# Kernel optimization log

Measured on AMD Instinct MI355X. Metric: run time of the kernel, lower is better.

Reference implementation:

```python
import jax, jax.numpy as jnp
import numpy as np

BLOCK = 128  # fp8 weight block size (128, 128)

def dequant_block_fp8(w, scale_inv, block=BLOCK):
    # w: [E, N, K] fp8 values (simulated in f32); scale_inv: [E, N//block, K//block]
    E, N, K = w.shape
    wb = w.reshape(E, N // block, block, K // block, block)
    wb = wb * scale_inv[:, :, None, :, None]
    return wb.reshape(E, N, K)

def setup_inputs() -> dict:
    E, T, H, I, TOPK = 8, 256, 2048, 1024, 2
    key = jax.random.key(0)
    ks = jax.random.split(key, 6)
    x = jax.random.normal(ks[0], (T, H), dtype=jnp.float32)
    topk_ids = jax.random.randint(ks[1], (T, TOPK), 0, E, dtype=jnp.int64)
    topk_weights = jax.random.uniform(ks[2], (T, TOPK), dtype=jnp.float32)
    # fused gate+up projection: [E, 2I, H]; down projection: [E, H, I]
    w13_fp8 = jax.random.normal(ks[3], (E, 2 * I, H), dtype=jnp.float32) * 0.05
    w13_scale = jax.random.uniform(ks[4], (E, 2 * I // BLOCK, H // BLOCK), dtype=jnp.float32, minval=0.5, maxval=1.5)
    w2_fp8 = jax.random.normal(ks[5], (E, H, I), dtype=jnp.float32) * 0.05
    w2_scale = jax.random.uniform(jax.random.fold_in(key, 7), (E, H // BLOCK, I // BLOCK), dtype=jnp.float32, minval=0.5, maxval=1.5)
    return {
        "x": x, "topk_ids": topk_ids, "topk_weights": topk_weights,
        "w13_fp8": w13_fp8, "w13_scale": w13_scale,
        "w2_fp8": w2_fp8, "w2_scale": w2_scale,
        "moe_n_slice": 1, "n_expert_slice": 8, "ep_shift": 0,
    }

def reference(x, topk_ids, topk_weights, w13_fp8, w13_scale, w2_fp8, w2_scale,
              moe_n_slice, n_expert_slice, ep_shift):
    T, H = x.shape
    E = w13_fp8.shape[0]
    I = w2_fp8.shape[2]
    # per-expert block-FP8 dequant (the redundant dequant the kernel should fuse)
    w13 = dequant_block_fp8(w13_fp8, w13_scale)  # [E, 2I, H]
    w2 = dequant_block_fp8(w2_fp8, w2_scale)     # [E, H, I]
    # SwiGLU expert MLP computed for all experts, combined by routing weights
    gate_up = jnp.einsum('th,enh->ten', x, w13)  # [T, E, 2I]
    gate, up = gate_up[..., :I], gate_up[..., I:]
    act = jax.nn.silu(gate) * up                 # [T, E, I]
    y = jnp.einsum('tei,ehi->teh', act, w2)      # [T, E, H]
    # dense combine matrix equivalent to routed top-k dispatch
    combine = jnp.zeros((T, E), x.dtype).at[jnp.arange(T)[:, None], topk_ids].add(topk_weights.astype(x.dtype))
    return jnp.einsum('teh,te->th', y, combine)
```

## Files before the change

kernel.cpp:

```cpp
#include <hip/hip_runtime.h>
#include <cstdint>

#define NEXP 8
#define NTOK 256
#define NSLOT 512
#define HD 2048
#define ID 1024

typedef short bf16x8 __attribute__((ext_vector_type(8)));
typedef float f32x4  __attribute__((ext_vector_type(4)));

__global__ __launch_bounds__(256) void route_k(const int* __restrict__ ids,
                                               int* __restrict__ counts,
                                               int* __restrict__ slots) {
  int tid = threadIdx.x;
  if (tid < NEXP) counts[tid] = 0;
  __syncthreads();
  for (int s = tid; s < NSLOT; s += 256) {
    int e = ids[s];
    int pos = atomicAdd(&counts[e], 1);
    slots[e * NSLOT + pos] = s;
  }
}

__device__ __forceinline__ void split4(float x, float y, float z, float w,
                                       uint2& hi, uint2& lo) {
  uint32_t u0 = __float_as_uint(x), u1 = __float_as_uint(y),
           u2 = __float_as_uint(z), u3 = __float_as_uint(w);
  uint32_t h0 = u0 & 0xFFFF0000u, h1 = u1 & 0xFFFF0000u;
  uint32_t h2 = u2 & 0xFFFF0000u, h3 = u3 & 0xFFFF0000u;
  hi.x = (u0 >> 16) | h1;
  hi.y = (u2 >> 16) | h3;
  float l0 = x - __uint_as_float(h0), l1 = y - __uint_as_float(h1);
  float l2 = z - __uint_as_float(h2), l3 = w - __uint_as_float(h3);
  lo.x = (__float_as_uint(l0) >> 16) | (__float_as_uint(l1) & 0xFFFF0000u);
  lo.y = (__float_as_uint(l2) >> 16) | (__float_as_uint(l3) & 0xFFFF0000u);
}

template <int K, int ASHIFT>
__global__ __launch_bounds__(256, 2) void moe_gemm_mfma(
    const float* __restrict__ A, int lda,
    const float* __restrict__ B, int64_t bstride,
    const float* __restrict__ Sc, int sstride_e, int sstride_n,
    float* __restrict__ C, int ldc,
    const int* __restrict__ counts, const int* __restrict__ slots) {
  constexpr int NT = K / 32;
  const int e = blockIdx.z;
  const int cnt = counts[e];
  const int mbase = blockIdx.y * 64;
  if (mbase >= cnt) return;
  const int n0 = blockIdx.x * 64;

  __shared__ ushort Ah[2][64][32], Al[2][64][32];
  __shared__ ushort Bh[2][64][32], Bl[2][64][32];
  __shared__ int s_slots[64];

  const int tid = threadIdx.x;
  const int lane = tid & 63;
  const int wave = tid >> 6;
  const int wm = wave >> 1;
  const int wn = wave & 1;

  const int* sl = slots + e * NSLOT;
  if (tid < 64) {
    int m = mbase + tid;
    s_slots[tid] = sl[m < cnt ? m : cnt - 1];
  }

  const int rs = tid >> 3;
  const int c4 = (tid & 7) << 2;

  int ma0 = mbase + rs;      ma0 = ma0 < cnt ? ma0 : cnt - 1;
  int ma1 = mbase + 32 + rs; ma1 = ma1 < cnt ? ma1 : cnt - 1;
  const float* ap0 = A + (int64_t)(sl[ma0] >> ASHIFT) * lda + c4;
  const float* ap1 = A + (int64_t)(sl[ma1] >> ASHIFT) * lda + c4;
  const float* Be  = B + (int64_t)e * bstride;
  const float* bp0 = Be + (int64_t)(n0 + rs) * K + c4;
  const float* bp1 = Be + (int64_t)(n0 + 32 + rs) * K + c4;
  const float* Se  = Sc + e * sstride_e + (n0 >> 7) * sstride_n;

  f32x4 acc[2][2] = {};

  float4 A0a, A1a, B0a, B1a;
  float4 A0b, A1b, B0b, B1b;

#define GLOAD(S, t)                                  \
  {                                                  \
    const int k0_ = (t) * 32;                        \
    A0##S = *(const float4*)(ap0 + k0_);             \
    A1##S = *(const float4*)(ap1 + k0_);             \
    B0##S = *(const float4*)(bp0 + k0_);             \
    B1##S = *(const float4*)(bp1 + k0_);             \
  }

  auto stage = [&](int buf, int tt, const float4& a0, const float4& a1,
                   const float4& b0, const float4& b1) {
    const float s = Se[tt >> 2];
    uint2 h, l;
    split4(a0.x, a0.y, a0.z, a0.w, h, l);
    *(uint2*)&Ah[buf][rs][c4] = h;       *(uint2*)&Al[buf][rs][c4] = l;
    split4(a1.x, a1.y, a1.z, a1.w, h, l);
    *(uint2*)&Ah[buf][rs + 32][c4] = h;  *(uint2*)&Al[buf][rs + 32][c4] = l;
    split4(b0.x * s, b0.y * s, b0.z * s, b0.w * s, h, l);
    *(uint2*)&Bh[buf][rs][c4] = h;       *(uint2*)&Bl[buf][rs][c4] = l;
    split4(b1.x * s, b1.y * s, b1.z * s, b1.w * s, h, l);
    *(uint2*)&Bh[buf][rs + 32][c4] = h;  *(uint2*)&Bl[buf][rs + 32][c4] = l;
  };

  auto do_mfma = [&](int buf) {
    if (mbase + (wm << 5) >= cnt) return;
    const int k8 = (lane >> 4) << 3;
    const int ar = (wm << 5) + (lane & 15);
    const int br = (wn << 5) + (lane & 15);
    bf16x8 ah[2], al2[2], bh[2], bl2[2];
#pragma unroll
    for (int i = 0; i < 2; ++i) {
      ah[i]  = *(const bf16x8*)&Ah[buf][ar + i * 16][k8];
      al2[i] = *(const bf16x8*)&Al[buf][ar + i * 16][k8];
      bh[i]  = *(const bf16x8*)&Bh[buf][br + i * 16][k8];
      bl2[i] = *(const bf16x8*)&Bl[buf][br + i * 16][k8];
    }
#pragma unroll
    for (int mf = 0; mf < 2; ++mf)
#pragma unroll
      for (int nf = 0; nf < 2; ++nf) {
        acc[mf][nf] = __builtin_amdgcn_mfma_f32_16x16x32_bf16(ah[mf],  bh[nf],  acc[mf][nf], 0, 0, 0);
        acc[mf][nf] = __builtin_amdgcn_mfma_f32_16x16x32_bf16(ah[mf],  bl2[nf], acc[mf][nf], 0, 0, 0);
        acc[mf][nf] = __builtin_amdgcn_mfma_f32_16x16x32_bf16(al2[mf], bh[nf],  acc[mf][nf], 0, 0, 0);
      }
  };

  GLOAD(a, 0)
  GLOAD(b, 1)
  stage(0, 0, A0a, A1a, B0a, B1a);
  __syncthreads();

  for (int t = 0; t < NT; t += 2) {
    if (t + 2 < NT) GLOAD(a, t + 2)
    do_mfma(0);
    stage(1, t + 1, A0b, A1b, B0b, B1b);
    __syncthreads();
    if (t + 3 < NT) GLOAD(b, t + 3)
    do_mfma(1);
    if (t + 2 < NT) stage(0, t + 2, A0a, A1a, B0a, B1a);
    __syncthreads();
  }
#undef GLOAD

#pragma unroll
  for (int mf = 0; mf < 2; ++mf) {
#pragma unroll
    for (int nf = 0; nf < 2; ++nf) {
      const int rbase = (wm << 5) + (mf << 4) + ((lane >> 4) << 2);
      const int col = n0 + (wn << 5) + (nf << 4) + (lane & 15);
#pragma unroll
      for (int r = 0; r < 4; ++r) {
        const int row = rbase + r;
        if (mbase + row < cnt)
          C[(int64_t)s_slots[row] * ldc + col] = acc[mf][nf][r];
      }
    }
  }
}

__global__ __launch_bounds__(256) void act_k(const float* __restrict__ gu,
                                             float* __restrict__ act) {
  int idx = blockIdx.x * 256 + threadIdx.x;
  int s  = idx >> 8;
  int i4 = (idx & 255) << 2;
  const float4 g = *(const float4*)(gu + (int64_t)s * (2 * ID) + i4);
  const float4 u = *(const float4*)(gu + (int64_t)s * (2 * ID) + ID + i4);
  float4 r;
  r.x = g.x / (1.f + expf(-g.x)) * u.x;
  r.y = g.y / (1.f + expf(-g.y)) * u.y;
  r.z = g.z / (1.f + expf(-g.z)) * u.z;
  r.w = g.w / (1.f + expf(-g.w)) * u.w;
  *(float4*)(act + (int64_t)s * ID + i4) = r;
}

__global__ __launch_bounds__(256) void combine_k(const float* __restrict__ y,
                                                 const float* __restrict__ wts,
                                                 float* __restrict__ out) {
  int idx = blockIdx.x * 256 + threadIdx.x;
  int t  = idx >> 9;
  int h4 = (idx & 511) << 2;
  float w0 = wts[t * 2], w1 = wts[t * 2 + 1];
  const float4 y0 = *(const float4*)(y + (int64_t)(2 * t) * HD + h4);
  const float4 y1 = *(const float4*)(y + (int64_t)(2 * t + 1) * HD + h4);
  float4 r;
  r.x = w0 * y0.x + w1 * y1.x;
  r.y = w0 * y0.y + w1 * y1.y;
  r.z = w0 * y0.z + w1 * y1.z;
  r.w = w0 * y0.w + w1 * y1.w;
  *(float4*)(out + (int64_t)t * HD + h4) = r;
}

extern "C" void kernel_launch(void* const* d_in, const int* in_sizes, int n_in,
                              void* d_out, int out_size, void* d_ws, size_t ws_size,
                              hipStream_t stream) {
  const float* x   = (const float*)d_in[0];
  const int*   ids = (const int*)d_in[1];
  const float* wts = (const float*)d_in[2];
  const float* w13 = (const float*)d_in[3];
  const float* s13 = (const float*)d_in[4];
  const float* w2  = (const float*)d_in[5];
  const float* s2  = (const float*)d_in[6];
  float* out = (float*)d_out;

  char* ws = (char*)d_ws;
  int* counts = (int*)ws;
  int* slots  = (int*)(ws + 64);
  float* gu   = (float*)(ws + 32768);
  float* act  = (float*)(ws + 32768 + (4u << 20));
  float* y    = (float*)(ws + 32768 + (6u << 20));

  route_k<<<1, 256, 0, stream>>>(ids, counts, slots);

  moe_gemm_mfma<HD, 1><<<dim3(32, 8, NEXP), 256, 0, stream>>>(
      x, HD,
      w13, (int64_t)(2 * ID) * HD,
      s13, (2 * ID / 128) * (HD / 128), HD / 128,
      gu, 2 * ID, counts, slots);

  act_k<<<512, 256, 0, stream>>>(gu, act);

  moe_gemm_mfma<ID, 0><<<dim3(32, 8, NEXP), 256, 0, stream>>>(
      act, ID,
      w2, (int64_t)HD * ID,
      s2, (HD / 128) * (ID / 128), ID / 128,
      y, HD, counts, slots);

  combine_k<<<512, 256, 0, stream>>>(y, wts, out);
}
```

Baseline: 337.8 us.

## Split-K both MoE GEMMs with atomic accumulation and fuse routing-weight combine

Both expert GEMMs now split the K dimension into four chunks across the grid's z axis and accumulate partial results with float atomicAdd. This gives four times as many blocks to fill the GPU when expert token counts are small. The second GEMM scales its output by the routing weight and atomically adds into the final output, which removes the separate combine kernel and the y buffer. The change also pads the LDS tiles to 40 columns to reduce bank conflicts and raises launch bounds occupancy to 3. In exchange it adds two zeroing kernels, heavy atomic traffic, and non-deterministic summation order.

```diff
diff --git a/kernel.cpp b/kernel.cpp
--- a/kernel.cpp
+++ b/kernel.cpp
@@ -21,6 +21,11 @@
     int pos = atomicAdd(&counts[e], 1);
     slots[e * NSLOT + pos] = s;
   }
+}
+
+__global__ __launch_bounds__(256) void zero_k(float4* __restrict__ p, int n4) {
+  int i = blockIdx.x * 256 + threadIdx.x;
+  if (i < n4) p[i] = make_float4(0.f, 0.f, 0.f, 0.f);
 }
 
 __device__ __forceinline__ void split4(float x, float y, float z, float w,
@@ -37,23 +42,28 @@
   lo.y = (__float_as_uint(l2) >> 16) | (__float_as_uint(l3) & 0xFFFF0000u);
 }
 
-template <int K, int ASHIFT>
-__global__ __launch_bounds__(256, 2) void moe_gemm_mfma(
+template <int K, int ASHIFT, int KS, bool FUSE>
+__global__ __launch_bounds__(256, 3) void moe_gemm_mfma(
     const float* __restrict__ A, int lda,
     const float* __restrict__ B, int64_t bstride,
     const float* __restrict__ Sc, int sstride_e, int sstride_n,
     float* __restrict__ C, int ldc,
+    const float* __restrict__ wts,
     const int* __restrict__ counts, const int* __restrict__ slots) {
   constexpr int NT = K / 32;
-  const int e = blockIdx.z;
+  constexpr int NTC = NT / KS;
+  const int e  = blockIdx.z / KS;
+  const int kc = blockIdx.z % KS;
   const int cnt = counts[e];
   const int mbase = blockIdx.y * 64;
   if (mbase >= cnt) return;
   const int n0 = blockIdx.x * 64;
-
-  __shared__ ushort Ah[2][64][32], Al[2][64][32];
-  __shared__ ushort Bh[2][64][32], Bl[2][64][32];
-  __shared__ int s_slots[64];
+  const int t0 = kc * NTC;
+
+  __shared__ ushort Ah[2][64][40], Al[2][64][40];
+  __shared__ ushort Bh[2][64][40], Bl[2][64][40];
+  __shared__ int   s_slots[64];
+  __shared__ float s_wts[64];
 
   const int tid = threadIdx.x;
   const int lane = tid & 63;
@@ -64,7 +74,9 @@
   const int* sl = slots + e * NSLOT;
   if (tid < 64) {
     int m = mbase + tid;
-    s_slots[tid] = sl[m < cnt ? m : cnt - 1];
+    int sv = sl[m < cnt ? m : cnt - 1];
+    s_slots[tid] = sv;
+    s_wts[tid] = FUSE ? wts[sv] : 0.f;
   }
 
   const int rs = tid >> 3;
@@ -130,19 +142,19 @@
       }
   };
 
-  GLOAD(a, 0)
-  GLOAD(b, 1)
-  stage(0, 0, A0a, A1a, B0a, B1a);
+  GLOAD(a, t0)
+  GLOAD(b, t0 + 1)
+  stage(0, t0, A0a, A1a, B0a, B1a);
   __syncthreads();
 
-  for (int t = 0; t < NT; t += 2) {
-    if (t + 2 < NT) GLOAD(a, t + 2)
+  for (int t = t0; t < t0 + NTC; t += 2) {
+    if (t + 2 < t0 + NTC) GLOAD(a, t + 2)
     do_mfma(0);
     stage(1, t + 1, A0b, A1b, B0b, B1b);
     __syncthreads();
-    if (t + 3 < NT) GLOAD(b, t + 3)
+    if (t + 3 < t0 + NTC) GLOAD(b, t + 3)
     do_mfma(1);
-    if (t + 2 < NT) stage(0, t + 2, A0a, A1a, B0a, B1a);
+    if (t + 2 < t0 + NTC) stage(0, t + 2, A0a, A1a, B0a, B1a);
     __syncthreads();
   }
 #undef GLOAD
@@ -156,8 +168,14 @@
 #pragma unroll
       for (int r = 0; r < 4; ++r) {
         const int row = rbase + r;
-        if (mbase + row < cnt)
-          C[(int64_t)s_slots[row] * ldc + col] = acc[mf][nf][r];
+        if (mbase + row < cnt) {
+          if (FUSE) {
+            atomicAdd(&C[(int64_t)(s_slots[row] >> 1) * ldc + col],
+                      acc[mf][nf][r] * s_wts[row]);
+          } else {
+            atomicAdd(&C[(int64_t)s_slots[row] * ldc + col], acc[mf][nf][r]);
+          }
+        }
       }
     }
   }
@@ -178,23 +196,6 @@
   *(float4*)(act + (int64_t)s * ID + i4) = r;
 }
 
-__global__ __launch_bounds__(256) void combine_k(const float* __restrict__ y,
-                                                 const float* __restrict__ wts,
-                                                 float* __restrict__ out) {
-  int idx = blockIdx.x * 256 + threadIdx.x;
-  int t  = idx >> 9;
-  int h4 = (idx & 511) << 2;
-  float w0 = wts[t * 2], w1 = wts[t * 2 + 1];
-  const float4 y0 = *(const float4*)(y + (int64_t)(2 * t) * HD + h4);
-  const float4 y1 = *(const float4*)(y + (int64_t)(2 * t + 1) * HD + h4);
-  float4 r;
-  r.x = w0 * y0.x + w1 * y1.x;
-  r.y = w0 * y0.y + w1 * y1.y;
-  r.z = w0 * y0.z + w1 * y1.z;
-  r.w = w0 * y0.w + w1 * y1.w;
-  *(float4*)(out + (int64_t)t * HD + h4) = r;
-}
-
 extern "C" void kernel_launch(void* const* d_in, const int* in_sizes, int n_in,
                               void* d_out, int out_size, void* d_ws, size_t ws_size,
                               hipStream_t stream) {
@@ -212,23 +213,22 @@
   int* slots  = (int*)(ws + 64);
   float* gu   = (float*)(ws + 32768);
   float* act  = (float*)(ws + 32768 + (4u << 20));
-  float* y    = (float*)(ws + 32768 + (6u << 20));
 
   route_k<<<1, 256, 0, stream>>>(ids, counts, slots);
-
-  moe_gemm_mfma<HD, 1><<<dim3(32, 8, NEXP), 256, 0, stream>>>(
+  zero_k<<<1024, 256, 0, stream>>>((float4*)gu, NSLOT * 2 * ID / 4);
+  zero_k<<<512, 256, 0, stream>>>((float4*)out, NTOK * HD / 4);
+
+  moe_gemm_mfma<HD, 1, 4, false><<<dim3(32, 8, NEXP * 4), 256, 0, stream>>>(
       x, HD,
       w13, (int64_t)(2 * ID) * HD,
       s13, (2 * ID / 128) * (HD / 128), HD / 128,
-      gu, 2 * ID, counts, slots);
+      gu, 2 * ID, nullptr, counts, slots);
 
   act_k<<<512, 256, 0, stream>>>(gu, act);
 
-  moe_gemm_mfma<ID, 0><<<dim3(32, 8, NEXP), 256, 0, stream>>>(
+  moe_gemm_mfma<ID, 0, 4, true><<<dim3(32, 8, NEXP * 4), 256, 0, stream>>>(
       act, ID,
       w2, (int64_t)HD * ID,
       s2, (HD / 128) * (ID / 128), ID / 128,
-      y, HD, counts, slots);
-
-  combine_k<<<512, 256, 0, stream>>>(y, wts, out);
-}
+      out, HD, wts, counts, slots);
+}
```

After: 285.9 us. -15.4%, faster.

## Split-K both MoE GEMMs into four partials reduced in act and combine kernels

Applied to the files above, without the earlier changes.

Both expert GEMMs are split along K into four chunks, with blockIdx.z encoding expert and chunk, so the grid is four times larger. Each chunk writes its own partial buffer, and the activation and combine kernels sum the four partials before applying SiLU or the routing weights. Shared tiles are padded to a row stride of 40 to cut LDS bank conflicts, per-chunk scales are preloaded into registers, the K loop is fully unrolled with explicit waitcnt and barriers, and occupancy is raised to three blocks. The cost is four times the intermediate write and read traffic and a larger workspace.

```diff
diff --git a/kernel.cpp b/kernel.cpp
--- a/kernel.cpp
+++ b/kernel.cpp
@@ -37,22 +37,27 @@
   lo.y = (__float_as_uint(l2) >> 16) | (__float_as_uint(l3) & 0xFFFF0000u);
 }
 
-template <int K, int ASHIFT>
-__global__ __launch_bounds__(256, 2) void moe_gemm_mfma(
+template <int K, int ASHIFT, int KS>
+__device__ __forceinline__ void gemm_body(
     const float* __restrict__ A, int lda,
     const float* __restrict__ B, int64_t bstride,
     const float* __restrict__ Sc, int sstride_e, int sstride_n,
     float* __restrict__ C, int ldc,
     const int* __restrict__ counts, const int* __restrict__ slots) {
   constexpr int NT = K / 32;
-  const int e = blockIdx.z;
+  constexpr int NTC = NT / KS;
+  constexpr int NSC = NTC / 4;
+  const int e  = blockIdx.z / KS;
+  const int kc = blockIdx.z % KS;
   const int cnt = counts[e];
   const int mbase = blockIdx.y * 64;
   if (mbase >= cnt) return;
   const int n0 = blockIdx.x * 64;
-
-  __shared__ ushort Ah[2][64][32], Al[2][64][32];
-  __shared__ ushort Bh[2][64][32], Bl[2][64][32];
+  const int t0 = kc * NTC;
+  float* Cpart = C + (int64_t)kc * NSLOT * ldc;
+
+  __shared__ ushort Ah[2][64][40], Al[2][64][40];
+  __shared__ ushort Bh[2][64][40], Bl[2][64][40];
   __shared__ int s_slots[64];
 
   const int tid = threadIdx.x;
@@ -72,42 +77,42 @@
 
   int ma0 = mbase + rs;      ma0 = ma0 < cnt ? ma0 : cnt - 1;
   int ma1 = mbase + 32 + rs; ma1 = ma1 < cnt ? ma1 : cnt - 1;
-  const float* ap0 = A + (int64_t)(sl[ma0] >> ASHIFT) * lda + c4;
-  const float* ap1 = A + (int64_t)(sl[ma1] >> ASHIFT) * lda + c4;
+  const float* ap0 = A + (int64_t)(sl[ma0] >> ASHIFT) * lda + t0 * 32 + c4;
+  const float* ap1 = A + (int64_t)(sl[ma1] >> ASHIFT) * lda + t0 * 32 + c4;
   const float* Be  = B + (int64_t)e * bstride;
-  const float* bp0 = Be + (int64_t)(n0 + rs) * K + c4;
-  const float* bp1 = Be + (int64_t)(n0 + 32 + rs) * K + c4;
-  const float* Se  = Sc + e * sstride_e + (n0 >> 7) * sstride_n;
+  const float* bp0 = Be + (int64_t)(n0 + rs) * K + t0 * 32 + c4;
+  const float* bp1 = Be + (int64_t)(n0 + 32 + rs) * K + t0 * 32 + c4;
+
+  float scl[NSC];
+  {
+    const float* Se = Sc + e * sstride_e + (n0 >> 7) * sstride_n + kc * NSC;
+#pragma unroll
+    for (int i = 0; i < NSC; ++i) scl[i] = Se[i];
+  }
 
   f32x4 acc[2][2] = {};
-
-  float4 A0a, A1a, B0a, B1a;
-  float4 A0b, A1b, B0b, B1b;
-
-#define GLOAD(S, t)                                  \
-  {                                                  \
-    const int k0_ = (t) * 32;                        \
-    A0##S = *(const float4*)(ap0 + k0_);             \
-    A1##S = *(const float4*)(ap1 + k0_);             \
-    B0##S = *(const float4*)(bp0 + k0_);             \
-    B1##S = *(const float4*)(bp1 + k0_);             \
-  }
-
-  auto stage = [&](int buf, int tt, const float4& a0, const float4& a1,
-                   const float4& b0, const float4& b1) {
-    const float s = Se[tt >> 2];
+  float4 rA0[2], rA1[2], rB0[2], rB1[2];
+
+  auto gload = [&](int s, int t) {
+    rA0[s] = *(const float4*)(ap0 + t * 32);
+    rA1[s] = *(const float4*)(ap1 + t * 32);
+    rB0[s] = *(const float4*)(bp0 + t * 32);
+    rB1[s] = *(const float4*)(bp1 + t * 32);
+  };
+
+  auto stage_s = [&](int s, int buf, float sc) {
     uint2 h, l;
-    split4(a0.x, a0.y, a0.z, a0.w, h, l);
+    split4(rA0[s].x, rA0[s].y, rA0[s].z, rA0[s].w, h, l);
     *(uint2*)&Ah[buf][rs][c4] = h;       *(uint2*)&Al[buf][rs][c4] = l;
-    split4(a1.x, a1.y, a1.z, a1.w, h, l);
+    split4(rA1[s].x, rA1[s].y, rA1[s].z, rA1[s].w, h, l);
     *(uint2*)&Ah[buf][rs + 32][c4] = h;  *(uint2*)&Al[buf][rs + 32][c4] = l;
-    split4(b0.x * s, b0.y * s, b0.z * s, b0.w * s, h, l);
+    split4(rB0[s].x * sc, rB0[s].y * sc, rB0[s].z * sc, rB0[s].w * sc, h, l);
     *(uint2*)&Bh[buf][rs][c4] = h;       *(uint2*)&Bl[buf][rs][c4] = l;
-    split4(b1.x * s, b1.y * s, b1.z * s, b1.w * s, h, l);
+    split4(rB1[s].x * sc, rB1[s].y * sc, rB1[s].z * sc, rB1[s].w * sc, h, l);
     *(uint2*)&Bh[buf][rs + 32][c4] = h;  *(uint2*)&Bl[buf][rs + 32][c4] = l;
   };
 
-  auto do_mfma = [&](int buf) {
+  auto mfma_step = [&](int buf) {
     if (mbase + (wm << 5) >= cnt) return;
     const int k8 = (lane >> 4) << 3;
     const int ar = (wm << 5) + (lane & 15);
@@ -130,22 +135,23 @@
       }
   };
 
-  GLOAD(a, 0)
-  GLOAD(b, 1)
-  stage(0, 0, A0a, A1a, B0a, B1a);
-  __syncthreads();
-
-  for (int t = 0; t < NT; t += 2) {
-    if (t + 2 < NT) GLOAD(a, t + 2)
-    do_mfma(0);
-    stage(1, t + 1, A0b, A1b, B0b, B1b);
-    __syncthreads();
-    if (t + 3 < NT) GLOAD(b, t + 3)
-    do_mfma(1);
-    if (t + 2 < NT) stage(0, t + 2, A0a, A1a, B0a, B1a);
-    __syncthreads();
-  }
-#undef GLOAD
+  gload(0, 0);
+  gload(1, 1);
+  stage_s(0, 0, scl[0]);
+  asm volatile("s_waitcnt lgkmcnt(0)" ::: "memory");
+  __builtin_amdgcn_s_barrier();
+
+#pragma unroll
+  for (int t = 0; t < NTC; ++t) {
+    const int buf = t & 1;
+    if (t + 2 < NTC) gload(buf, t + 2);
+    mfma_step(buf);
+    if (t + 1 < NTC) {
+      stage_s((t + 1) & 1, (t + 1) & 1, scl[(t + 1) >> 2]);
+      asm volatile("s_waitcnt lgkmcnt(0)" ::: "memory");
+      __builtin_amdgcn_s_barrier();
+    }
+  }
 
 #pragma unroll
   for (int mf = 0; mf < 2; ++mf) {
@@ -157,19 +163,45 @@
       for (int r = 0; r < 4; ++r) {
         const int row = rbase + r;
         if (mbase + row < cnt)
-          C[(int64_t)s_slots[row] * ldc + col] = acc[mf][nf][r];
+          Cpart[(int64_t)s_slots[row] * ldc + col] = acc[mf][nf][r];
       }
     }
   }
 }
 
-__global__ __launch_bounds__(256) void act_k(const float* __restrict__ gu,
+__global__ __launch_bounds__(256, 3) void gemm1_k(
+    const float* __restrict__ A, const float* __restrict__ B,
+    const float* __restrict__ Sc, float* __restrict__ C,
+    const int* __restrict__ counts, const int* __restrict__ slots) {
+  gemm_body<HD, 1, 4>(A, HD, B, (int64_t)(2 * ID) * HD,
+                      Sc, (2 * ID / 128) * (HD / 128), HD / 128,
+                      C, 2 * ID, counts, slots);
+}
+
+__global__ __launch_bounds__(256, 3) void gemm2_k(
+    const float* __restrict__ A, const float* __restrict__ B,
+    const float* __restrict__ Sc, float* __restrict__ C,
+    const int* __restrict__ counts, const int* __restrict__ slots) {
+  gemm_body<ID, 0, 4>(A, ID, B, (int64_t)HD * ID,
+                      Sc, (HD / 128) * (ID / 128), ID / 128,
+                      C, HD, counts, slots);
+}
+
+__global__ __launch_bounds__(256) void act_k(const float* __restrict__ gup,
                                              float* __restrict__ act) {
   int idx = blockIdx.x * 256 + threadIdx.x;
   int s  = idx >> 8;
   int i4 = (idx & 255) << 2;
-  const float4 g = *(const float4*)(gu + (int64_t)s * (2 * ID) + i4);
-  const float4 u = *(const float4*)(gu + (int64_t)s * (2 * ID) + ID + i4);
+  float4 g = make_float4(0.f, 0.f, 0.f, 0.f);
+  float4 u = make_float4(0.f, 0.f, 0.f, 0.f);
+#pragma unroll
+  for (int kc = 0; kc < 4; ++kc) {
+    const float* p = gup + ((int64_t)kc * NSLOT + s) * (2 * ID);
+    const float4 gv = *(const float4*)(p + i4);
+    const float4 uv = *(const float4*)(p + ID + i4);
+    g.x += gv.x; g.y += gv.y; g.z += gv.z; g.w += gv.w;
+    u.x += uv.x; u.y += uv.y; u.z += uv.z; u.w += uv.w;
+  }
   float4 r;
   r.x = g.x / (1.f + expf(-g.x)) * u.x;
   r.y = g.y / (1.f + expf(-g.y)) * u.y;
@@ -178,15 +210,23 @@
   *(float4*)(act + (int64_t)s * ID + i4) = r;
 }
 
-__global__ __launch_bounds__(256) void combine_k(const float* __restrict__ y,
+__global__ __launch_bounds__(256) void combine_k(const float* __restrict__ yp,
                                                  const float* __restrict__ wts,
                                                  float* __restrict__ out) {
   int idx = blockIdx.x * 256 + threadIdx.x;
   int t  = idx >> 9;
   int h4 = (idx & 511) << 2;
   float w0 = wts[t * 2], w1 = wts[t * 2 + 1];
-  const float4 y0 = *(const float4*)(y + (int64_t)(2 * t) * HD + h4);
-  const float4 y1 = *(const float4*)(y + (int64_t)(2 * t + 1) * HD + h4);
+  float4 y0 = make_float4(0.f, 0.f, 0.f, 0.f);
+  float4 y1 = make_float4(0.f, 0.f, 0.f, 0.f);
+#pragma unroll
+  for (int kc = 0; kc < 4; ++kc) {
+    const float* p0 = yp + ((int64_t)kc * NSLOT + 2 * t) * HD;
+    const float4 a = *(const float4*)(p0 + h4);
+    const float4 b = *(const float4*)(p0 + HD + h4);
+    y0.x += a.x; y0.y += a.y; y0.z += a.z; y0.w += a.w;
+    y1.x += b.x; y1.y += b.y; y1.z += b.z; y1.w += b.w;
+  }
   float4 r;
   r.x = w0 * y0.x + w1 * y1.x;
   r.y = w0 * y0.y + w1 * y1.y;
@@ -208,27 +248,21 @@
   float* out = (float*)d_out;
 
   char* ws = (char*)d_ws;
-  int* counts = (int*)ws;
-  int* slots  = (int*)(ws + 64);
-  float* gu   = (float*)(ws + 32768);
-  float* act  = (float*)(ws + 32768 + (4u << 20));
-  float* y    = (float*)(ws + 32768 + (6u << 20));
+  int* counts    = (int*)ws;
+  int* slots     = (int*)(ws + 64);
+  float* gu_part = (float*)(ws + 32768);
+  float* act     = (float*)(ws + 32768 + (16u << 20));
+  float* y_part  = (float*)(ws + 32768 + (18u << 20));
 
   route_k<<<1, 256, 0, stream>>>(ids, counts, slots);
 
-  moe_gemm_mfma<HD, 1><<<dim3(32, 8, NEXP), 256, 0, stream>>>(
-      x, HD,
-      w13, (int64_t)(2 * ID) * HD,
-      s13, (2 * ID / 128) * (HD / 128), HD / 128,
-      gu, 2 * ID, counts, slots);
-
-  act_k<<<512, 256, 0, stream>>>(gu, act);
-
-  moe_gemm_mfma<ID, 0><<<dim3(32, 8, NEXP), 256, 0, stream>>>(
-      act, ID,
-      w2, (int64_t)HD * ID,
-      s2, (HD / 128) * (ID / 128), ID / 128,
-      y, HD, counts, slots);
-
-  combine_k<<<512, 256, 0, stream>>>(y, wts, out);
-}
+  gemm1_k<<<dim3(32, 8, NEXP * 4), 256, 0, stream>>>(
+      x, w13, s13, gu_part, counts, slots);
+
+  act_k<<<512, 256, 0, stream>>>(gu_part, act);
+
+  gemm2_k<<<dim3(32, 8, NEXP * 4), 256, 0, stream>>>(
+      act, w2, s2, y_part, counts, slots);
+
+  combine_k<<<512, 256, 0, stream>>>(y_part, wts, out);
+}
```

New measurement: 282.2 us. 1.2x faster.
